# Optimization experiments

Hardware: AMD Instinct MI355X
Metric: run time of the kernel (lower is better)

## Reference

```python
import jax, jax.numpy as jnp
import numpy as np

B, LQ, LK, D = 16, 2048, 2048, 64
EPS = 1e-13
KEEP_PROB = 0.8  # fraction of key positions kept in the mask


def setup_inputs() -> dict:
    key = jax.random.key(0)
    kq, kk, kv, km = jax.random.split(key, 4)
    q = jax.random.normal(kq, (B, LQ, D), dtype=jnp.float32)
    k = jax.random.normal(kk, (B, LK, D), dtype=jnp.float32)
    v = jax.random.normal(kv, (B, LK, D), dtype=jnp.float32)
    # binary 0/1 float mask over key positions (ESIM-style padding mask)
    v_mask = (jax.random.uniform(km, (B, LK)) < KEEP_PROB).astype(jnp.float32)
    return {"q": q, "k": k, "v": v, "v_mask": v_mask}


def masked_softmax(scores, mask):
    # ESIM masked_softmax: softmax(scores * mask) * mask, renormalized.
    m = mask[:, None, :]  # [B, 1, Lk] broadcast over query dim
    p = jax.nn.softmax(scores * m, axis=-1) * m
    return p / (jnp.sum(p, axis=-1, keepdims=True) + EPS)


def reference(q, k, v, v_mask):
    scores = jnp.einsum("bqd,bkd->bqk", q, k)  # [B, Lq, Lk]
    attend = masked_softmax(scores, v_mask)
    return jnp.einsum("bqk,bkd->bqd", attend, v)  # [B, Lq, D]
```

## Files before the change

### kernel.cpp

```cpp
#include <hip/hip_runtime.h>
#include <hip/hip_bf16.h>
#include <stdint.h>

#define NB 16
#define SLQ 2048
#define SLK 2048
#define DD 64
#define BQ 128
#define BK 64
#define NT (SLK / BK)
#define QTILES (SLQ / BQ)
#define LOG2E 1.44269504f

typedef _Float16 f16x8 __attribute__((ext_vector_type(8)));
typedef short s16x8 __attribute__((ext_vector_type(8)));
typedef unsigned int u32x4 __attribute__((ext_vector_type(4)));
typedef unsigned short u16x4 __attribute__((ext_vector_type(4)));
typedef float f32x4 __attribute__((ext_vector_type(4)));
typedef float f32x2 __attribute__((ext_vector_type(2)));
typedef float f32x16 __attribute__((ext_vector_type(16)));

typedef __attribute__((address_space(1))) const void gvoid;
typedef __attribute__((address_space(3))) void lvoid;

__device__ __forceinline__ int swzb(int row, int bytecol) {
    return row * 128 + (bytecol ^ ((row & 7) << 4));
}
__device__ __forceinline__ int ldsq(int row, int bytecol) {
    return (row >> 6) * 8192 + swzb(row & 63, bytecol);
}

__device__ __forceinline__ void gload16(const void* g, void* l) {
    __builtin_amdgcn_global_load_lds((gvoid*)g, (lvoid*)l, 16, 0, 0);
}
__device__ __forceinline__ void gload4(const void* g, void* l) {
    __builtin_amdgcn_global_load_lds((gvoid*)g, (lvoid*)l, 4, 0, 0);
}

__device__ __forceinline__ uint16_t f2bf(float f) {
    __bf16 h = (__bf16)f;
    return __builtin_bit_cast(uint16_t, h);
}
__device__ __forceinline__ float bf2f(uint16_t u) {
    uint32_t x = ((uint32_t)u) << 16;
    return __builtin_bit_cast(float, x);
}

__device__ __forceinline__ int sigma16(int x) {
    return (x & ~12) | ((x & 4) << 1) | ((x & 8) >> 1);
}

__device__ __forceinline__ void build_pa(const f32x16& s, s16x8& paA, s16x8& paB) {
    uint32_t w[8];
    #pragma unroll
    for (int i = 0; i < 8; ++i) {
        float p0 = exp2f(s[2 * i]);
        float p1 = exp2f(s[2 * i + 1]);
        w[i] = (uint32_t)f2bf(p0) | ((uint32_t)f2bf(p1) << 16);
    }
    u32x4 wa = {w[0], w[1], w[2], w[3]};
    u32x4 wb = {w[4], w[5], w[6], w[7]};
    paA = __builtin_bit_cast(s16x8, wa);
    paB = __builtin_bit_cast(s16x8, wb);
}

__global__ __launch_bounds__(256)
void prep_all(const float* __restrict__ q, const float* __restrict__ k,
              const float* __restrict__ v, const float* __restrict__ vm,
              char* __restrict__ qs, char* __restrict__ ks,
              char* __restrict__ vts, uint16_t* __restrict__ mb16) {
    const int bid = blockIdx.x;
    if (bid < 1024) {
        const int tl = bid & 511;
        const bool isq = bid < 512;
        const float sc = isq ? LOG2E : 1.0f;
        const float* src = (isq ? q : k) + (size_t)tl * (BK * DD);
        char* dst = (isq ? qs : ks) + (size_t)tl * (BK * DD * 2);
        #pragma unroll
        for (int it = 0; it < 2; ++it) {
            int c = threadIdx.x + it * 256;
            int row = c >> 3, col8 = c & 7;
            f32x4 a  = *(const f32x4*)(src + row * DD + col8 * 8);
            f32x4 b2 = *(const f32x4*)(src + row * DD + col8 * 8 + 4);
            f16x8 h;
            #pragma unroll
            for (int j = 0; j < 4; ++j) {
                h[j] = (_Float16)(a[j] * sc);
                h[4 + j] = (_Float16)(b2[j] * sc);
            }
            *(f16x8*)(dst + swzb(row, col8 * 16)) = h;
        }
    } else if (bid < 1536) {
        const int tl = bid - 1024;
        const float* src = v + (size_t)tl * (BK * DD);
        const float* msk = vm + (size_t)tl * BK;
        char* dst = vts + (size_t)tl * (BK * DD * 2);
        const int d = threadIdx.x & 63;
        #pragma unroll
        for (int it = 0; it < 2; ++it) {
            int key8 = (threadIdx.x >> 6) + it * 4;
            s16x8 h;
            #pragma unroll
            for (int j = 0; j < 8; ++j) {
                int kp = key8 * 8 + j;
                int sk = (kp & ~15) | sigma16(kp & 15);
                float mv = msk[sk];
                h[j] = (short)f2bf((mv != 0.f) ? src[sk * DD + d] : 0.f);
            }
            *(s16x8*)(dst + swzb(d, key8 * 16)) = h;
        }
    } else {
        int i = (bid - 1536) * 1024 + threadIdx.x * 4;
        f32x4 m = *(const f32x4*)(vm + i);
        u16x4 o;
        #pragma unroll
        for (int j = 0; j < 4; ++j) o[j] = (m[j] != 0.f) ? (uint16_t)0x3F80 : (uint16_t)0;
        int pos = (i & ~15) | sigma16(i & 15);
        *(u16x4*)(mb16 + pos) = o;
    }
}

__global__ __launch_bounds__(256, 3)
void attn_fwd(const char* __restrict__ qs, const char* __restrict__ ks,
              const char* __restrict__ vts, const uint16_t* __restrict__ mb16,
              uint16_t* __restrict__ po, float* __restrict__ pl,
              float* __restrict__ out, int nsp)
{
    __shared__ __align__(16) char bufs[3][16640];

    const int tid  = threadIdx.x;
    const int lane = tid & 63;
    const int w    = tid >> 6;
    const int lh   = lane >> 5;
    const int lr   = lane & 31;

    const int G = 256 * nsp;
    int wg = blockIdx.x;
    wg = (wg & 7) * (G >> 3) + (wg >> 3);
    const int qt   = wg & 15;
    const int rest = wg >> 4;
    const int sp   = rest % nsp;
    const int b    = rest / nsp;

    const int qq = NT / nsp, rm = NT % nsp;
    const int t0  = sp * qq + (sp < rm ? sp : rm);
    const int cnt = qq + (sp < rm ? 1 : 0);

    const char* qtile = qs  + (size_t)(b * 32 + qt * 2) * 8192;
    const char* kbase = ks  + (size_t)(b * 32 + t0) * 8192;
    const char* vbase = vts + (size_t)(b * 32 + t0) * 8192;
    const uint16_t* mkbase = mb16 + (size_t)b * SLK + t0 * BK;

#define STAGE(kt, bf) do {                                                      \
        const char* kg_ = kbase + (size_t)(kt) * 8192;                          \
        const char* vg_ = vbase + (size_t)(kt) * 8192;                          \
        _Pragma("unroll")                                                       \
        for (int i_ = 0; i_ < 2; ++i_) {                                        \
            int ch_ = w * 2 + i_;                                               \
            gload16(kg_ + ch_ * 1024 + lane * 16, bufs[bf] + ch_ * 1024);       \
            gload16(vg_ + ch_ * 1024 + lane * 16, bufs[bf] + 8192 + ch_ * 1024);\
        }                                                                       \
        gload4((const char*)(mkbase + (size_t)(kt) * BK) + (lane & 31) * 4,     \
               bufs[bf] + 16384);                                               \
    } while (0)

    #pragma unroll
    for (int i = 0; i < 4; ++i) {
        int ch = w * 4 + i;
        gload16(qtile + ch * 1024 + lane * 16, bufs[2] + ch * 1024);
    }
    STAGE(0, 0);
    if (cnt > 1) {
        STAGE(1, 1);
        asm volatile("s_waitcnt vmcnt(5)" ::: "memory");
    } else {
        asm volatile("s_waitcnt vmcnt(0)" ::: "memory");
    }
    __builtin_amdgcn_s_barrier();

    f16x8 qf[4];
    #pragma unroll
    for (int kd = 0; kd < 4; ++kd)
        qf[kd] = *(const f16x8*)(bufs[2] + ldsq(w * 32 + lr, kd * 32 + lh * 16));
    asm volatile("s_waitcnt lgkmcnt(0)" ::: "memory");
    __builtin_amdgcn_s_barrier();

    f32x16 oacc0 = (f32x16)(0.0f), oacc1 = (f32x16)(0.0f), rsacc = (f32x16)(0.0f);

    for (int t = 0; t < cnt; ++t) {
        const int cur = t % 3;
        if (t + 2 < cnt) {
            STAGE(t + 2, (t + 2) % 3);
            asm volatile("s_waitcnt vmcnt(10)" ::: "memory");
        } else if (t + 1 < cnt) {
            asm volatile("s_waitcnt vmcnt(5)" ::: "memory");
        } else {
            asm volatile("s_waitcnt vmcnt(0)" ::: "memory");
        }
        __builtin_amdgcn_s_barrier();

        const char* kb_ = bufs[cur];
        const char* vb_ = bufs[cur] + 8192;
        const char* mb_ = bufs[cur] + 16384;

        s16x8 mf[4];
        #pragma unroll
        for (int kk = 0; kk < 4; ++kk)
            mf[kk] = *(const s16x8*)(mb_ + kk * 32 + lh * 16);

        __builtin_amdgcn_s_setprio(1);
        f32x16 s0 = (f32x16)(0.0f), s1 = (f32x16)(0.0f);
        #pragma unroll
        for (int kd = 0; kd < 4; ++kd) {
            f16x8 kf0 = *(const f16x8*)(kb_ + swzb(lr,      kd * 32 + lh * 16));
            f16x8 kf1 = *(const f16x8*)(kb_ + swzb(32 + lr, kd * 32 + lh * 16));
            s0 = __builtin_amdgcn_mfma_f32_32x32x16_f16(kf0, qf[kd], s0, 0, 0, 0);
            s1 = __builtin_amdgcn_mfma_f32_32x32x16_f16(kf1, qf[kd], s1, 0, 0, 0);
        }
        __builtin_amdgcn_s_setprio(0);

        s16x8 pa[4];
        build_pa(s0, pa[0], pa[1]);
        build_pa(s1, pa[2], pa[3]);

        __builtin_amdgcn_s_setprio(1);
        #pragma unroll
        for (int kk = 0; kk < 4; ++kk)
            rsacc = __builtin_amdgcn_mfma_f32_32x32x16_bf16(pa[kk], mf[kk], rsacc, 0, 0, 0);
        #pragma unroll
        for (int kk = 0; kk < 4; ++kk) {
            s16x8 vf0 = *(const s16x8*)(vb_ + swzb(lr,      kk * 32 + lh * 16));
            s16x8 vf1 = *(const s16x8*)(vb_ + swzb(32 + lr, kk * 32 + lh * 16));
            oacc0 = __builtin_amdgcn_mfma_f32_32x32x16_bf16(pa[kk], vf0, oacc0, 0, 0, 0);
            oacc1 = __builtin_amdgcn_mfma_f32_32x32x16_bf16(pa[kk], vf1, oacc1, 0, 0, 0);
        }
        __builtin_amdgcn_s_setprio(0);

        asm volatile("s_waitcnt lgkmcnt(0)" ::: "memory");
        __builtin_amdgcn_s_barrier();
    }
#undef STAGE

    if (nsp == 1) {
        float* ob = out + ((size_t)b * SLQ + (size_t)qt * BQ) * DD;
        #pragma unroll
        for (int r = 0; r < 16; ++r) {
            int row = w * 32 + (r & 3) + 8 * (r >> 2) + 4 * lh;
            float inv = 1.f / (rsacc[r] + 1e-13f);
            ob[row * DD + lr]      = oacc0[r] * inv;
            ob[row * DD + 32 + lr] = oacc1[r] * inv;
        }
    } else {
        uint16_t* pob = po + (size_t)wg * (BQ * DD);
        #pragma unroll
        for (int r = 0; r < 16; ++r) {
            int row = w * 32 + (r & 3) + 8 * (r >> 2) + 4 * lh;
            pob[row * DD + lr]      = f2bf(oacc0[r]);
            pob[row * DD + 32 + lr] = f2bf(oacc1[r]);
            if (lr == 0) pl[(size_t)wg * BQ + row] = rsacc[r];
        }
    }
}

__global__ __launch_bounds__(256)
void merge_k(const uint16_t* __restrict__ po, const float* __restrict__ pl,
             float* __restrict__ out, int nsp) {
    const int t  = blockIdx.x;
    const int b  = t >> 4, qt = t & 15;
    const int i0 = (b * nsp) * 16 + qt;
    const int r0 = threadIdx.x >> 4;
    const int c4 = (threadIdx.x & 15) * 4;
    float* ob = out + ((size_t)b * SLQ + (size_t)qt * BQ) * DD;
    for (int rr = 0; rr < BQ; rr += 16) {
        int r = r0 + rr;
        float l = 1e-13f;
        f32x4 acc = (f32x4){0.f, 0.f, 0.f, 0.f};
        for (int s = 0; s < nsp; ++s) {
            int idx = i0 + s * 16;
            l += pl[(size_t)idx * BQ + r];
            u16x4 a = *(const u16x4*)(po + (size_t)idx * (BQ * DD) + r * DD + c4);
            #pragma unroll
            for (int j = 0; j < 4; ++j) acc[j] += bf2f(a[j]);
        }
        float inv = 1.f / l;
        f32x4 o;
        #pragma unroll
        for (int j = 0; j < 4; ++j) o[j] = acc[j] * inv;
        *(f32x4*)(ob + r * DD + c4) = o;
    }
}

__global__ __launch_bounds__(256, 2)
void attn_fallback(const float* __restrict__ q, const float* __restrict__ k,
                   const float* __restrict__ v, const float* __restrict__ vm,
                   float* __restrict__ out)
{
    __shared__ __align__(16) char lqh[64 * DD * 2];
    __shared__ __align__(16) char lql[64 * DD * 2];
    __shared__ __align__(16) char lkh[BK * DD * 2];
    __shared__ __align__(16) char lkl[BK * DD * 2];
    __shared__ __align__(16) char lvt[DD * BK * 2];
    __shared__ __align__(16) char lpp[64 * BK * 2];
    __shared__ float lmask[BK];

    const int tid  = threadIdx.x;
    const int lane = tid & 63;
    const int w    = tid >> 6;
    const int lg   = lane >> 4;
    const int lm   = lane & 15;

    const int b  = blockIdx.y;
    const int qt = blockIdx.x;

    const float* qb = q + ((size_t)b * SLQ + (size_t)qt * 64) * DD;
    const float* kb = k + (size_t)b * SLK * DD;
    const float* vb = v + (size_t)b * SLK * DD;
    const float* mb = vm + (size_t)b * SLK;

    #pragma unroll
    for (int it = 0; it < 2; ++it) {
        int c = tid + it * 256;
        int row = c >> 3, col8 = c & 7;
        f32x4 a  = *(const f32x4*)(qb + row * DD + col8 * 8);
        f32x4 bb = *(const f32x4*)(qb + row * DD + col8 * 8 + 4);
        s16x8 h, l;
        #pragma unroll
        for (int j = 0; j < 4; ++j) {
            uint16_t hh = f2bf(a[j]);
            h[j] = (short)hh; l[j] = (short)f2bf(a[j] - bf2f(hh));
            uint16_t hb = f2bf(bb[j]);
            h[4 + j] = (short)hb; l[4 + j] = (short)f2bf(bb[j] - bf2f(hb));
        }
        *(s16x8*)(lqh + swzb(row, col8 * 16)) = h;
        *(s16x8*)(lql + swzb(row, col8 * 16)) = l;
    }
    __syncthreads();

    s16x8 qfh[2], qfl[2];
    #pragma unroll
    for (int kc = 0; kc < 2; ++kc) {
        qfh[kc] = *(const s16x8*)(lqh + swzb(w * 16 + lm, kc * 64 + lg * 16));
        qfl[kc] = *(const s16x8*)(lql + swzb(w * 16 + lm, kc * 64 + lg * 16));
    }

    float mrow[4], lrow[4];
    f32x4 oacc[4];
    #pragma unroll
    for (int i = 0; i < 4; ++i) { mrow[i] = -1e30f; lrow[i] = 0.f; }
    #pragma unroll
    for (int d = 0; d < 4; ++d) oacc[d] = (f32x4){0.f, 0.f, 0.f, 0.f};

    for (int kt = 0; kt < NT; ++kt) {
        __syncthreads();
        const float* ks2 = kb + (size_t)kt * BK * DD;
        const float* vs = vb + (size_t)kt * BK * DD;

        #pragma unroll
        for (int it = 0; it < 2; ++it) {
            int c = tid + it * 256;
            int row = c >> 3, col8 = c & 7;
            f32x4 a  = *(const f32x4*)(ks2 + row * DD + col8 * 8);
            f32x4 bb = *(const f32x4*)(ks2 + row * DD + col8 * 8 + 4);
            s16x8 h, l;
            #pragma unroll
            for (int j = 0; j < 4; ++j) {
                uint16_t hh = f2bf(a[j]);
                h[j] = (short)hh; l[j] = (short)f2bf(a[j] - bf2f(hh));
                uint16_t hb = f2bf(bb[j]);
                h[4 + j] = (short)hb; l[4 + j] = (short)f2bf(bb[j] - bf2f(hb));
            }
            *(s16x8*)(lkh + swzb(row, col8 * 16)) = h;
            *(s16x8*)(lkl + swzb(row, col8 * 16)) = l;
        }
        #pragma unroll
        for (int it = 0; it < 8; ++it) {
            int c = tid + it * 256;
            int key = c >> 5, dp = (c & 31) * 2;
            f32x2 a = *(const f32x2*)(vs + key * DD + dp);
            *(uint16_t*)(lvt + swzb(dp,     key * 2)) = f2bf(a[0]);
            *(uint16_t*)(lvt + swzb(dp + 1, key * 2)) = f2bf(a[1]);
        }
        if (tid < BK) lmask[tid] = mb[kt * BK + tid];
        __syncthreads();

        f32x4 s[4];
        #pragma unroll
        for (int f = 0; f < 4; ++f) s[f] = (f32x4){0.f, 0.f, 0.f, 0.f};
        #pragma unroll
        for (int f = 0; f < 4; ++f) {
            #pragma unroll
            for (int kc = 0; kc < 2; ++kc) {
                s16x8 kfh = *(const s16x8*)(lkh + swzb(f * 16 + lm, kc * 64 + lg * 16));
                s16x8 kfl = *(const s16x8*)(lkl + swzb(f * 16 + lm, kc * 64 + lg * 16));
                s[f] = __builtin_amdgcn_mfma_f32_16x16x32_bf16(qfh[kc], kfh, s[f], 0, 0, 0);
                s[f] = __builtin_amdgcn_mfma_f32_16x16x32_bf16(qfh[kc], kfl, s[f], 0, 0, 0);
                s[f] = __builtin_amdgcn_mfma_f32_16x16x32_bf16(qfl[kc], kfh, s[f], 0, 0, 0);
            }
        }

        float mv[4];
        #pragma unroll
        for (int f = 0; f < 4; ++f) mv[f] = lmask[f * 16 + lm];

        float pmax[4];
        #pragma unroll
        for (int i = 0; i < 4; ++i) {
            float x = -1e30f;
            #pragma unroll
            for (int f = 0; f < 4; ++f) {
                float sv = (mv[f] != 0.f) ? s[f][i] : -1e30f;
                s[f][i] = sv;
                x = fmaxf(x, sv);
            }
            #pragma unroll
            for (int off = 1; off < 16; off <<= 1)
                x = fmaxf(x, __shfl_xor(x, off, 64));
            pmax[i] = x;
        }

        float scl[4];
        #pragma unroll
        for (int i = 0; i < 4; ++i) {
            float mn = fmaxf(mrow[i], pmax[i]);
            scl[i] = __expf(mrow[i] - mn);
            mrow[i] = mn;
        }
        float rs[4] = {0.f, 0.f, 0.f, 0.f};
        #pragma unroll
        for (int f = 0; f < 4; ++f) {
            #pragma unroll
            for (int i = 0; i < 4; ++i) {
                float p = __expf(s[f][i] - mrow[i]);
                s[f][i] = p;
                rs[i] += p;
            }
        }
        #pragma unroll
        for (int i = 0; i < 4; ++i) {
            #pragma unroll
            for (int off = 1; off < 16; off <<= 1)
                rs[i] += __shfl_xor(rs[i], off, 64);
            lrow[i] = lrow[i] * scl[i] + rs[i];
        }
        #pragma unroll
        for (int d = 0; d < 4; ++d)
            #pragma unroll
            for (int i = 0; i < 4; ++i)
                oacc[d][i] *= scl[i];

        #pragma unroll
        for (int f = 0; f < 4; ++f)
            #pragma unroll
            for (int i = 0; i < 4; ++i)
                *(uint16_t*)(lpp + swzb(w * 16 + lg * 4 + i, (f * 16 + lm) * 2)) = f2bf(s[f][i]);
        __syncthreads();

        #pragma unroll
        for (int kc = 0; kc < 2; ++kc) {
            s16x8 pf = *(const s16x8*)(lpp + swzb(w * 16 + lm, kc * 64 + lg * 16));
            #pragma unroll
            for (int d = 0; d < 4; ++d) {
                s16x8 vf = *(const s16x8*)(lvt + swzb(d * 16 + lm, kc * 64 + lg * 16));
                oacc[d] = __builtin_amdgcn_mfma_f32_16x16x32_bf16(pf, vf, oacc[d], 0, 0, 0);
            }
        }
    }

    float* ob = out + ((size_t)b * SLQ + (size_t)qt * 64) * DD;
    #pragma unroll
    for (int i = 0; i < 4; ++i) {
        float inv = 1.f / (lrow[i] + 1e-13f);
        int row = w * 16 + lg * 4 + i;
        #pragma unroll
        for (int d = 0; d < 4; ++d)
            ob[row * DD + d * 16 + lm] = oacc[d][i] * inv;
    }
}

extern "C" void kernel_launch(void* const* d_in, const int* in_sizes, int n_in,
                              void* d_out, int out_size, void* d_ws, size_t ws_size,
                              hipStream_t stream) {
    const float* q  = (const float*)d_in[0];
    const float* k  = (const float*)d_in[1];
    const float* v  = (const float*)d_in[2];
    const float* vm = (const float*)d_in[3];
    float* out = (float*)d_out;

    const size_t TB     = (size_t)NB * SLK * DD * 2;
    const size_t MB     = (size_t)NB * SLK * 2;
    const size_t PL_PER = (size_t)NB * QTILES * BQ * 4;
    const size_t PO_PER = (size_t)NB * QTILES * BQ * DD * 2;
    const size_t base = 3 * TB + MB;

    int nsp = 0;
    for (int c = 3; c >= 1; --c) {
        if (ws_size >= base + (size_t)c * (PL_PER + PO_PER)) { nsp = c; break; }
    }
    if (nsp == 0) {
        if (ws_size >= base) nsp = 1;
        else {
            dim3 grid(SLQ / 64, NB);
            attn_fallback<<<grid, dim3(256), 0, stream>>>(q, k, v, vm, out);
            return;
        }
    }

    char*     qs   = (char*)d_ws;
    char*     ks   = qs + TB;
    char*     vts  = ks + TB;
    uint16_t* mb16 = (uint16_t*)(vts + TB);
    float*    pl   = (float*)((char*)mb16 + MB);
    uint16_t* po   = (uint16_t*)((char*)pl + (size_t)nsp * PL_PER);

    prep_all<<<dim3(1568), dim3(256), 0, stream>>>(q, k, v, vm, qs, ks, vts, mb16);
    attn_fwd<<<dim3(256 * nsp), dim3(256), 0, stream>>>(qs, ks, vts, mb16, po, pl, out, nsp);
    if (nsp > 1)
        merge_k<<<dim3(NB * QTILES), dim3(256), 0, stream>>>(po, pl, out, nsp);
}
```

Baseline: 58.66 us.

## Use double buffering, process key tile in halves, raise occupancy and split count

Shrinks the LDS staging from three buffers to two, which drops the prefetch depth to one tile ahead. The S/P computation is restructured to handle the 64-key tile in two 32-key halves, which lowers live register pressure (one score accumulator and two P fragments instead of four). Launch bounds go from 3 to 4 blocks per CU, and the host allows up to four key splits, trading a shallower prefetch pipeline and a larger split-combine for more resident waves and parallelism.

Result: no change. 59.67 us (+1.7%).

```diff
diff --git a/kernel.cpp b/kernel.cpp
--- a/kernel.cpp
+++ b/kernel.cpp
@@ -120,13 +120,13 @@
     }
 }
 
-__global__ __launch_bounds__(256, 3)
+__global__ __launch_bounds__(256, 4)
 void attn_fwd(const char* __restrict__ qs, const char* __restrict__ ks,
               const char* __restrict__ vts, const uint16_t* __restrict__ mb16,
               uint16_t* __restrict__ po, float* __restrict__ pl,
               float* __restrict__ out, int nsp)
 {
-    __shared__ __align__(16) char bufs[3][16640];
+    __shared__ __align__(16) char bufs[2][16640];
 
     const int tid  = threadIdx.x;
     const int lane = tid & 63;
@@ -167,32 +167,25 @@
     #pragma unroll
     for (int i = 0; i < 4; ++i) {
         int ch = w * 4 + i;
-        gload16(qtile + ch * 1024 + lane * 16, bufs[2] + ch * 1024);
+        gload16(qtile + ch * 1024 + lane * 16, bufs[1] + ch * 1024);
     }
     STAGE(0, 0);
-    if (cnt > 1) {
-        STAGE(1, 1);
-        asm volatile("s_waitcnt vmcnt(5)" ::: "memory");
-    } else {
-        asm volatile("s_waitcnt vmcnt(0)" ::: "memory");
-    }
+    asm volatile("s_waitcnt vmcnt(5)" ::: "memory");
     __builtin_amdgcn_s_barrier();
 
     f16x8 qf[4];
     #pragma unroll
     for (int kd = 0; kd < 4; ++kd)
-        qf[kd] = *(const f16x8*)(bufs[2] + ldsq(w * 32 + lr, kd * 32 + lh * 16));
+        qf[kd] = *(const f16x8*)(bufs[1] + ldsq(w * 32 + lr, kd * 32 + lh * 16));
     asm volatile("s_waitcnt lgkmcnt(0)" ::: "memory");
     __builtin_amdgcn_s_barrier();
 
     f32x16 oacc0 = (f32x16)(0.0f), oacc1 = (f32x16)(0.0f), rsacc = (f32x16)(0.0f);
 
     for (int t = 0; t < cnt; ++t) {
-        const int cur = t % 3;
-        if (t + 2 < cnt) {
-            STAGE(t + 2, (t + 2) % 3);
-            asm volatile("s_waitcnt vmcnt(10)" ::: "memory");
-        } else if (t + 1 < cnt) {
+        const int cur = t & 1;
+        if (t + 1 < cnt) {
+            STAGE(t + 1, cur ^ 1);
             asm volatile("s_waitcnt vmcnt(5)" ::: "memory");
         } else {
             asm volatile("s_waitcnt vmcnt(0)" ::: "memory");
@@ -203,38 +196,37 @@
         const char* vb_ = bufs[cur] + 8192;
         const char* mb_ = bufs[cur] + 16384;
 
-        s16x8 mf[4];
-        #pragma unroll
-        for (int kk = 0; kk < 4; ++kk)
-            mf[kk] = *(const s16x8*)(mb_ + kk * 32 + lh * 16);
-
-        __builtin_amdgcn_s_setprio(1);
-        f32x16 s0 = (f32x16)(0.0f), s1 = (f32x16)(0.0f);
-        #pragma unroll
-        for (int kd = 0; kd < 4; ++kd) {
-            f16x8 kf0 = *(const f16x8*)(kb_ + swzb(lr,      kd * 32 + lh * 16));
-            f16x8 kf1 = *(const f16x8*)(kb_ + swzb(32 + lr, kd * 32 + lh * 16));
-            s0 = __builtin_amdgcn_mfma_f32_32x32x16_f16(kf0, qf[kd], s0, 0, 0, 0);
-            s1 = __builtin_amdgcn_mfma_f32_32x32x16_f16(kf1, qf[kd], s1, 0, 0, 0);
-        }
-        __builtin_amdgcn_s_setprio(0);
-
-        s16x8 pa[4];
-        build_pa(s0, pa[0], pa[1]);
-        build_pa(s1, pa[2], pa[3]);
-
-        __builtin_amdgcn_s_setprio(1);
-        #pragma unroll
-        for (int kk = 0; kk < 4; ++kk)
-            rsacc = __builtin_amdgcn_mfma_f32_32x32x16_bf16(pa[kk], mf[kk], rsacc, 0, 0, 0);
-        #pragma unroll
-        for (int kk = 0; kk < 4; ++kk) {
-            s16x8 vf0 = *(const s16x8*)(vb_ + swzb(lr,      kk * 32 + lh * 16));
-            s16x8 vf1 = *(const s16x8*)(vb_ + swzb(32 + lr, kk * 32 + lh * 16));
-            oacc0 = __builtin_amdgcn_mfma_f32_32x32x16_bf16(pa[kk], vf0, oacc0, 0, 0, 0);
-            oacc1 = __builtin_amdgcn_mfma_f32_32x32x16_bf16(pa[kk], vf1, oacc1, 0, 0, 0);
-        }
-        __builtin_amdgcn_s_setprio(0);
+        #pragma unroll
+        for (int st = 0; st < 2; ++st) {
+            f32x16 s = (f32x16)(0.0f);
+            __builtin_amdgcn_s_setprio(1);
+            #pragma unroll
+            for (int kd = 0; kd < 4; ++kd) {
+                f16x8 kf = *(const f16x8*)(kb_ + swzb(st * 32 + lr, kd * 32 + lh * 16));
+                s = __builtin_amdgcn_mfma_f32_32x32x16_f16(kf, qf[kd], s, 0, 0, 0);
+            }
+            __builtin_amdgcn_s_setprio(0);
+
+            s16x8 pa0, pa1;
+            build_pa(s, pa0, pa1);
+
+            s16x8 mf0 = *(const s16x8*)(mb_ + st * 64 + lh * 16);
+            s16x8 mf1 = *(const s16x8*)(mb_ + st * 64 + 32 + lh * 16);
+
+            __builtin_amdgcn_s_setprio(1);
+            rsacc = __builtin_amdgcn_mfma_f32_32x32x16_bf16(pa0, mf0, rsacc, 0, 0, 0);
+            rsacc = __builtin_amdgcn_mfma_f32_32x32x16_bf16(pa1, mf1, rsacc, 0, 0, 0);
+
+            s16x8 vl0 = *(const s16x8*)(vb_ + swzb(lr,      st * 64 + lh * 16));
+            s16x8 vh0 = *(const s16x8*)(vb_ + swzb(32 + lr, st * 64 + lh * 16));
+            oacc0 = __builtin_amdgcn_mfma_f32_32x32x16_bf16(pa0, vl0, oacc0, 0, 0, 0);
+            oacc1 = __builtin_amdgcn_mfma_f32_32x32x16_bf16(pa0, vh0, oacc1, 0, 0, 0);
+            s16x8 vl1 = *(const s16x8*)(vb_ + swzb(lr,      st * 64 + 32 + lh * 16));
+            s16x8 vh1 = *(const s16x8*)(vb_ + swzb(32 + lr, st * 64 + 32 + lh * 16));
+            oacc0 = __builtin_amdgcn_mfma_f32_32x32x16_bf16(pa1, vl1, oacc0, 0, 0, 0);
+            oacc1 = __builtin_amdgcn_mfma_f32_32x32x16_bf16(pa1, vh1, oacc1, 0, 0, 0);
+            __builtin_amdgcn_s_setprio(0);
+        }
 
         asm volatile("s_waitcnt lgkmcnt(0)" ::: "memory");
         __builtin_amdgcn_s_barrier();
@@ -493,7 +485,7 @@
     const size_t base = 3 * TB + MB;
 
     int nsp = 0;
-    for (int c = 3; c >= 1; --c) {
+    for (int c = 4; c >= 1; --c) {
         if (ws_size >= base + (size_t)c * (PL_PER + PO_PER)) { nsp = c; break; }
     }
     if (nsp == 0) {
```
